# Kernel optimization log

Hardware: AMD Instinct MI355X
Metric: run time of the kernel (lower is better)

Reference implementation:

```python
import jax, jax.numpy as jnp
import numpy as np

B, T, N, FIN, FOUT, EDGE_DIM = 8, 16, 256, 32, 32, 16


def setup_inputs() -> dict:
    key = jax.random.key(0)
    ks = jax.random.split(key, 8)
    def xavier(k, shape):
        fan_in, fan_out = shape[0], shape[1]
        limit = float(np.sqrt(6.0 / (fan_in + fan_out)))
        return jax.random.uniform(k, shape, jnp.float32, -limit, limit)
    return {
        "x": jax.random.normal(ks[0], (B, T, N, FIN), jnp.float32),
        "adj": jax.random.uniform(ks[1], (N, N), jnp.float32),
        # edge_net: Linear(1, edge_dim) -> GELU -> Linear(edge_dim, Fin*Fout)
        "w1": xavier(ks[2], (1, EDGE_DIM)),
        "b1": jnp.zeros((EDGE_DIM,), jnp.float32),
        "w2": xavier(ks[3], (EDGE_DIM, FIN * FOUT)),
        "b2": jnp.zeros((FIN * FOUT,), jnp.float32),
        # node_lin: Linear(Fin, Fout)
        "node_w": xavier(ks[4], (FIN, FOUT)),
        "node_b": jnp.zeros((FOUT,), jnp.float32),
    }


def reference(x, adj, w1, b1, w2, b2, node_w, node_b):
    # edge-conditioned weights: (N, N, Fin, Fout)
    h = jax.nn.gelu(adj[:, :, None] * w1[0] + b1, approximate=False)  # (N,N,E)
    edge_w = (h @ w2 + b2).reshape(N, N, FIN, FOUT)
    # msg[b,t,i,j,:] = sum_f x[b,t,j,f] * edge_w[i,j,f,:]; agg = sum_j msg
    agg = jnp.einsum("btjf,ijfo->btio", x, edge_w)  # (B,T,N,Fout)
    y = jax.nn.gelu(x @ node_w + node_b + agg, approximate=False)
    return y
```

## Files before the change

kernel.cpp:

```cpp
#include <hip/hip_runtime.h>
#include <math.h>

#define NB    256
#define EDIM  16
#define FINN  32
#define FOUTN 32
#define BT    128
#define KKD   4096

typedef __attribute__((ext_vector_type(8))) short short8;
typedef __attribute__((ext_vector_type(4))) float floatx4;

#define MFMA16(a,b,c) __builtin_amdgcn_mfma_f32_16x16x32_bf16((a),(b),(c),0,0,0)

__device__ __forceinline__ float gelu_f(float v) {
    return 0.5f * v * (1.0f + erff(v * 0.70710678118654752f));
}
__device__ __forceinline__ ushort f2bf(float x) {
    union { float f; unsigned u; } v; v.f = x;
    unsigned r = (v.u + 0x7FFFu + ((v.u >> 16) & 1u)) >> 16;
    return (ushort)r;
}
__device__ __forceinline__ float bf2f(ushort b) {
    union { unsigned u; float f; } v; v.u = ((unsigned)b) << 16; return v.f;
}

__global__ __launch_bounds__(256) void h_kernel(const float* __restrict__ adj,
                                                const float* __restrict__ w1,
                                                const float* __restrict__ b1,
                                                ushort* __restrict__ H) {
    int i   = blockIdx.x;
    int tid = threadIdx.x;
    int e   = tid >> 4;
    int seg = tid & 15;
    float w = w1[e], b = b1[e];
    const float4* arow = (const float4*)(adj + (size_t)i * NB + seg * 16);
    ushort tmp[16];
    #pragma unroll
    for (int q = 0; q < 4; ++q) {
        float4 a = arow[q];
        tmp[q*4+0] = f2bf(gelu_f(a.x * w + b));
        tmp[q*4+1] = f2bf(gelu_f(a.y * w + b));
        tmp[q*4+2] = f2bf(gelu_f(a.z * w + b));
        tmp[q*4+3] = f2bf(gelu_f(a.w * w + b));
    }
    int4* dst = (int4*)(H + (size_t)i * KKD + e * 256 + seg * 16);
    dst[0] = *(int4*)&tmp[0];
    dst[1] = *(int4*)&tmp[8];
}

#define CH   512
#define NCH  8
#define BSP  520
#define XBP  40

__global__ __launch_bounds__(256, 1) void fused_kernel(
        const float* __restrict__ x,      const float* __restrict__ w2,
        const float* __restrict__ b2,     const float* __restrict__ node_w,
        const float* __restrict__ node_b, const ushort* __restrict__ H,
        float* __restrict__ out) {
    __shared__ ushort xb[NB][XBP];
    __shared__ ushort Bs[2][32][BSP];
    __shared__ ushort nwT[32][XBP];
    __shared__ float  Sp[8][32];
    __shared__ float  Sv[32];
    __shared__ float  bias2[32];

    int bt    = blockIdx.x;
    int ihalf = blockIdx.y;
    int tid   = threadIdx.x;
    int wv    = tid >> 6;
    int lane  = tid & 63;
    int m     = lane & 15;
    int quad  = lane >> 4;

    const float4* xg = (const float4*)(x + (size_t)bt * NB * FINN);
    #pragma unroll
    for (int it = 0; it < 8; ++it) {
        int idx4 = it * 256 + tid;
        float4 v = xg[idx4];
        int j = idx4 >> 3, f = (idx4 & 7) * 4;
        unsigned lo = (unsigned)f2bf(v.x) | ((unsigned)f2bf(v.y) << 16);
        unsigned hi = (unsigned)f2bf(v.z) | ((unsigned)f2bf(v.w) << 16);
        uint2 p; p.x = lo; p.y = hi;
        *(uint2*)&xb[j][f] = p;
    }
    {
        float4 v = ((const float4*)node_w)[tid];
        int f = tid >> 3, o = (tid & 7) * 4;
        nwT[o + 0][f] = f2bf(v.x); nwT[o + 1][f] = f2bf(v.y);
        nwT[o + 2][f] = f2bf(v.z); nwT[o + 3][f] = f2bf(v.w);
    }
    __syncthreads();

    {
        int f = tid & 31, grp = tid >> 5;
        float s = 0.f;
        for (int j = grp * 32; j < grp * 32 + 32; ++j) s += bf2f(xb[j][f]);
        Sp[grp][f] = s;
    }

    short8 afr[16];
    #pragma unroll
    for (int jt = 0; jt < 16; ++jt)
        afr[jt] = *(short8*)&xb[jt * 16 + m][quad * 8];
    int eoff = wv & 1;
    int ot   = wv >> 1;
    short8 wfr[NCH];
    #pragma unroll
    for (int c = 0; c < NCH; ++c) {
        int e = 2 * c + eoff;
        const float* wp = w2 + (size_t)e * (FINN * FOUTN)
                          + (quad * 8) * FOUTN + ot * 16 + m;
        short8 bb;
        #pragma unroll
        for (int i = 0; i < 8; ++i) bb[i] = (short)f2bf(wp[i * FOUTN]);
        wfr[c] = bb;
    }
    __syncthreads();
    if (tid < 32) {
        float s = 0.f;
        #pragma unroll
        for (int g = 0; g < 8; ++g) s += Sp[g][tid];
        Sv[tid] = s;
    }

    floatx4 acc[2][2] = {};
    int i0g = ihalf * 128 + wv * 32;

    #define Y2CHUNK(c, buf)                                                   \
    {                                                                         \
        short8 wb = wfr[c];                                                   \
        _Pragma("unroll")                                                     \
        for (int jt = 0; jt < 16; ++jt) {                                     \
            floatx4 z = {0.f, 0.f, 0.f, 0.f};                                 \
            floatx4 d = MFMA16(afr[jt], wb, z);                               \
            unsigned lo = (unsigned)f2bf(d[0]) | ((unsigned)f2bf(d[1]) << 16);\
            unsigned hi = (unsigned)f2bf(d[2]) | ((unsigned)f2bf(d[3]) << 16);\
            uint2 pv; pv.x = lo; pv.y = hi;                                   \
            *(uint2*)&Bs[buf][ot * 16 + m][eoff * 256 + jt * 16 + quad * 4] = pv; \
        }                                                                     \
    }

    Y2CHUNK(0, 0);
    __syncthreads();
    if (tid < 32) {
        float bb = node_b[tid];
        #pragma unroll
        for (int f = 0; f < FINN; ++f) bb += Sv[f] * b2[f * FOUTN + tid];
        bias2[tid] = bb;
    }

    #pragma unroll
    for (int c = 0; c < NCH; ++c) {
        if (c < NCH - 1) {
            if (c + 1 == 1) Y2CHUNK(1, 1);
            if (c + 1 == 2) Y2CHUNK(2, 0);
            if (c + 1 == 3) Y2CHUNK(3, 1);
            if (c + 1 == 4) Y2CHUNK(4, 0);
            if (c + 1 == 5) Y2CHUNK(5, 1);
            if (c + 1 == 6) Y2CHUNK(6, 0);
            if (c + 1 == 7) Y2CHUNK(7, 1);
        }
        const int buf = c & 1;
        #pragma unroll
        for (int kk = 0; kk < CH; kk += 32) {
            int kg = c * CH + kk + quad * 8;
            short8 a0 = *(const short8*)(H + (size_t)(i0g +      m) * KKD + kg);
            short8 a1 = *(const short8*)(H + (size_t)(i0g + 16 + m) * KKD + kg);
            short8 b0 = *(short8*)&Bs[buf][     m][kk + quad * 8];
            short8 b1 = *(short8*)&Bs[buf][16 + m][kk + quad * 8];
            acc[0][0] = MFMA16(a0, b0, acc[0][0]);
            acc[0][1] = MFMA16(a0, b1, acc[0][1]);
            acc[1][0] = MFMA16(a1, b0, acc[1][0]);
            acc[1][1] = MFMA16(a1, b1, acc[1][1]);
        }
        __syncthreads();
    }

    #pragma unroll
    for (int tm = 0; tm < 2; ++tm) {
        short8 xa = *(short8*)&xb[i0g + tm * 16 + m][quad * 8];
        #pragma unroll
        for (int tn = 0; tn < 2; ++tn) {
            short8 nb = *(short8*)&nwT[tn * 16 + m][quad * 8];
            acc[tm][tn] = MFMA16(xa, nb, acc[tm][tn]);
        }
    }
    #pragma unroll
    for (int tm = 0; tm < 2; ++tm)
        #pragma unroll
        for (int tn = 0; tn < 2; ++tn) {
            int o = tn * 16 + m;
            float bz = bias2[o];
            #pragma unroll
            for (int r = 0; r < 4; ++r) {
                int row = i0g + tm * 16 + quad * 4 + r;
                out[((size_t)bt * NB + row) * FOUTN + o] =
                    gelu_f(acc[tm][tn][r] + bz);
            }
        }
}

extern "C" void kernel_launch(void* const* d_in, const int* in_sizes, int n_in,
                              void* d_out, int out_size, void* d_ws, size_t ws_size,
                              hipStream_t stream) {
    const float* x      = (const float*)d_in[0];
    const float* adj    = (const float*)d_in[1];
    const float* w1     = (const float*)d_in[2];
    const float* b1     = (const float*)d_in[3];
    const float* w2     = (const float*)d_in[4];
    const float* b2     = (const float*)d_in[5];
    const float* node_w = (const float*)d_in[6];
    const float* node_b = (const float*)d_in[7];
    float* out = (float*)d_out;

    ushort* H = (ushort*)d_ws;

    hipLaunchKernelGGL(h_kernel, dim3(NB), dim3(256), 0, stream,
                       adj, w1, b1, H);
    hipLaunchKernelGGL(fused_kernel, dim3(BT, 2), dim3(256), 0, stream,
                       x, w2, b2, node_w, node_b, H, out);
}
```

Measured before the change: 111.4 us.

## Split rows into quarters with smaller K chunks for two blocks per CU

Doubles the grid along the output-row dimension so each block handles 64 rows, halves the K chunk size, and reduces the shared B buffer so two blocks fit per CU. w2 fragments are now loaded per chunk instead of held in registers, and each wave produces its own slice of the Y2 tile. This aims to raise occupancy and latency hiding, at the cost of recomputing the x·w2 product in twice as many blocks.

Result: no change. 112.0 us (+0.5%).

```diff
diff --git a/kernel.cpp b/kernel.cpp
--- a/kernel.cpp
+++ b/kernel.cpp
@@ -49,12 +49,12 @@
     dst[1] = *(int4*)&tmp[8];
 }
 
-#define CH   512
-#define NCH  8
-#define BSP  520
+#define CH   256
+#define NCH  16
+#define BSP  264
 #define XBP  40
 
-__global__ __launch_bounds__(256, 1) void fused_kernel(
+__global__ __launch_bounds__(256, 2) void fused_kernel(
         const float* __restrict__ x,      const float* __restrict__ w2,
         const float* __restrict__ b2,     const float* __restrict__ node_w,
         const float* __restrict__ node_b, const ushort* __restrict__ H,
@@ -66,13 +66,13 @@
     __shared__ float  Sv[32];
     __shared__ float  bias2[32];
 
-    int bt    = blockIdx.x;
-    int ihalf = blockIdx.y;
-    int tid   = threadIdx.x;
-    int wv    = tid >> 6;
-    int lane  = tid & 63;
-    int m     = lane & 15;
-    int quad  = lane >> 4;
+    int bt   = blockIdx.x;
+    int iq   = blockIdx.y;
+    int tid  = threadIdx.x;
+    int wv   = tid >> 6;
+    int lane = tid & 63;
+    int m    = lane & 15;
+    int quad = lane >> 4;
 
     const float4* xg = (const float4*)(x + (size_t)bt * NB * FINN);
     #pragma unroll
@@ -100,23 +100,11 @@
         Sp[grp][f] = s;
     }
 
-    short8 afr[16];
-    #pragma unroll
-    for (int jt = 0; jt < 16; ++jt)
-        afr[jt] = *(short8*)&xb[jt * 16 + m][quad * 8];
-    int eoff = wv & 1;
-    int ot   = wv >> 1;
-    short8 wfr[NCH];
-    #pragma unroll
-    for (int c = 0; c < NCH; ++c) {
-        int e = 2 * c + eoff;
-        const float* wp = w2 + (size_t)e * (FINN * FOUTN)
-                          + (quad * 8) * FOUTN + ot * 16 + m;
-        short8 bb;
-        #pragma unroll
-        for (int i = 0; i < 8; ++i) bb[i] = (short)f2bf(wp[i * FOUTN]);
-        wfr[c] = bb;
-    }
+    short8 afr[4];
+    #pragma unroll
+    for (int t = 0; t < 4; ++t)
+        afr[t] = *(short8*)&xb[(wv * 4 + t) * 16 + m][quad * 8];
+
     __syncthreads();
     if (tid < 32) {
         float s = 0.f;
@@ -125,24 +113,41 @@
         Sv[tid] = s;
     }
 
-    floatx4 acc[2][2] = {};
-    int i0g = ihalf * 128 + wv * 32;
-
-    #define Y2CHUNK(c, buf)                                                   \
+    floatx4 acc[2] = {};
+    int i0g = iq * 64 + wv * 16;
+
+    #define WLOAD(e, d0, d1)                                                  \
     {                                                                         \
-        short8 wb = wfr[c];                                                   \
+        const float* wp = w2 + (size_t)(e) * (FINN * FOUTN)                   \
+                          + (quad * 8) * FOUTN + m;                           \
         _Pragma("unroll")                                                     \
-        for (int jt = 0; jt < 16; ++jt) {                                     \
+        for (int i = 0; i < 8; ++i) {                                         \
+            d0[i] = (short)f2bf(wp[i * FOUTN]);                               \
+            d1[i] = (short)f2bf(wp[i * FOUTN + 16]);                          \
+        }                                                                     \
+    }
+
+    #define PRODUCE(buf, wa, wb)                                              \
+    {                                                                         \
+        _Pragma("unroll")                                                     \
+        for (int t = 0; t < 4; ++t) {                                         \
             floatx4 z = {0.f, 0.f, 0.f, 0.f};                                 \
-            floatx4 d = MFMA16(afr[jt], wb, z);                               \
-            unsigned lo = (unsigned)f2bf(d[0]) | ((unsigned)f2bf(d[1]) << 16);\
-            unsigned hi = (unsigned)f2bf(d[2]) | ((unsigned)f2bf(d[3]) << 16);\
-            uint2 pv; pv.x = lo; pv.y = hi;                                   \
-            *(uint2*)&Bs[buf][ot * 16 + m][eoff * 256 + jt * 16 + quad * 4] = pv; \
+            floatx4 d0 = MFMA16(afr[t], wa, z);                               \
+            floatx4 d1 = MFMA16(afr[t], wb, z);                               \
+            int col = (wv * 4 + t) * 16 + quad * 4;                           \
+            uint2 p0, p1;                                                     \
+            p0.x = (unsigned)f2bf(d0[0]) | ((unsigned)f2bf(d0[1]) << 16);     \
+            p0.y = (unsigned)f2bf(d0[2]) | ((unsigned)f2bf(d0[3]) << 16);     \
+            p1.x = (unsigned)f2bf(d1[0]) | ((unsigned)f2bf(d1[1]) << 16);     \
+            p1.y = (unsigned)f2bf(d1[2]) | ((unsigned)f2bf(d1[3]) << 16);     \
+            *(uint2*)&Bs[buf][     m][col] = p0;                              \
+            *(uint2*)&Bs[buf][16 + m][col] = p1;                              \
         }                                                                     \
     }
 
-    Y2CHUNK(0, 0);
+    short8 wc0, wc1;
+    WLOAD(0, wc0, wc1);
+    PRODUCE(0, wc0, wc1);
     __syncthreads();
     if (tid < 32) {
         float bb = node_b[tid];
@@ -154,52 +159,40 @@
     #pragma unroll
     for (int c = 0; c < NCH; ++c) {
         if (c < NCH - 1) {
-            if (c + 1 == 1) Y2CHUNK(1, 1);
-            if (c + 1 == 2) Y2CHUNK(2, 0);
-            if (c + 1 == 3) Y2CHUNK(3, 1);
-            if (c + 1 == 4) Y2CHUNK(4, 0);
-            if (c + 1 == 5) Y2CHUNK(5, 1);
-            if (c + 1 == 6) Y2CHUNK(6, 0);
-            if (c + 1 == 7) Y2CHUNK(7, 1);
-        }
-        const int buf = c & 1;
+            short8 wn0, wn1;
+            WLOAD(c + 1, wn0, wn1);
+            PRODUCE((c + 1) & 1, wn0, wn1);
+        }
+        const ushort* Hrow0 = H + (size_t)(i0g + m) * KKD + c * CH;
         #pragma unroll
         for (int kk = 0; kk < CH; kk += 32) {
-            int kg = c * CH + kk + quad * 8;
-            short8 a0 = *(const short8*)(H + (size_t)(i0g +      m) * KKD + kg);
-            short8 a1 = *(const short8*)(H + (size_t)(i0g + 16 + m) * KKD + kg);
-            short8 b0 = *(short8*)&Bs[buf][     m][kk + quad * 8];
-            short8 b1 = *(short8*)&Bs[buf][16 + m][kk + quad * 8];
-            acc[0][0] = MFMA16(a0, b0, acc[0][0]);
-            acc[0][1] = MFMA16(a0, b1, acc[0][1]);
-            acc[1][0] = MFMA16(a1, b0, acc[1][0]);
-            acc[1][1] = MFMA16(a1, b1, acc[1][1]);
+            short8 a0 = *(const short8*)(Hrow0 + kk + quad * 8);
+            short8 b0 = *(short8*)&Bs[c & 1][     m][kk + quad * 8];
+            short8 b1 = *(short8*)&Bs[c & 1][16 + m][kk + quad * 8];
+            acc[0] = MFMA16(a0, b0, acc[0]);
+            acc[1] = MFMA16(a0, b1, acc[1]);
         }
         __syncthreads();
     }
 
-    #pragma unroll
-    for (int tm = 0; tm < 2; ++tm) {
-        short8 xa = *(short8*)&xb[i0g + tm * 16 + m][quad * 8];
+    {
+        short8 xa = *(short8*)&xb[i0g + m][quad * 8];
         #pragma unroll
         for (int tn = 0; tn < 2; ++tn) {
             short8 nb = *(short8*)&nwT[tn * 16 + m][quad * 8];
-            acc[tm][tn] = MFMA16(xa, nb, acc[tm][tn]);
-        }
-    }
-    #pragma unroll
-    for (int tm = 0; tm < 2; ++tm)
-        #pragma unroll
-        for (int tn = 0; tn < 2; ++tn) {
-            int o = tn * 16 + m;
-            float bz = bias2[o];
-            #pragma unroll
-            for (int r = 0; r < 4; ++r) {
-                int row = i0g + tm * 16 + quad * 4 + r;
-                out[((size_t)bt * NB + row) * FOUTN + o] =
-                    gelu_f(acc[tm][tn][r] + bz);
-            }
-        }
+            acc[tn] = MFMA16(xa, nb, acc[tn]);
+        }
+    }
+    #pragma unroll
+    for (int tn = 0; tn < 2; ++tn) {
+        int o = tn * 16 + m;
+        float bz = bias2[o];
+        #pragma unroll
+        for (int r = 0; r < 4; ++r) {
+            int row = i0g + quad * 4 + r;
+            out[((size_t)bt * NB + row) * FOUTN + o] = gelu_f(acc[tn][r] + bz);
+        }
+    }
 }
 
 extern "C" void kernel_launch(void* const* d_in, const int* in_sizes, int n_in,
@@ -219,6 +212,6 @@
 
     hipLaunchKernelGGL(h_kernel, dim3(NB), dim3(256), 0, stream,
                        adj, w1, b1, H);
-    hipLaunchKernelGGL(fused_kernel, dim3(BT, 2), dim3(256), 0, stream,
+    hipLaunchKernelGGL(fused_kernel, dim3(BT, 4), dim3(256), 0, stream,
                        x, w2, b2, node_w, node_b, H, out);
 }
```
